# Optimization experiments

Measured on AMD Instinct MI355X. Metric: run time of the kernel, lower is better.

The kernel has to match this reference:

```python
import jax, jax.numpy as jnp
import numpy as np

B, NX, NY, NZ = 2, 64, 64, 64
D, CI, CO, F = 3, 32, 32, 64  # spatial dims, chan in/out, n_modes


def setup_inputs() -> dict:
    key = jax.random.key(0)
    ka, kx, ky, k1, k2, k3, k4, k5, k6 = jax.random.split(key, 9)
    omega, c = 30.0 / 300.0, 6.0
    u = lambda k, shape, scale: scale * (2.0 * jax.random.uniform(k, shape, jnp.float32) - 1.0)
    return {
        "a": jax.random.normal(ka, (B, NX, NY, NZ, CI), jnp.float32),
        "x": jax.random.uniform(kx, (B, NX, NY, NZ, D), jnp.float32),
        "y": jax.random.uniform(ky, (B, NX, NY, NZ, D), jnp.float32),
        "modes_a": u(k1, (F, CI), np.sqrt(c / (CI + F))),
        "modes_x": u(k2, (F, D), np.sqrt(c / (D + F)) * omega),
        "modes_y": u(k3, (F, D), np.sqrt(c / (D + F)) * omega),
        "modes_u": u(k4, (F, CO), np.sqrt(c / (F + CO))),
        "fc_w": jax.random.normal(k5, (CI, CO), jnp.float32) / np.sqrt(CI),
        "fc_b": jax.random.normal(k6, (CO,), jnp.float32) * 0.01,
    }


def reference(a, x, y, modes_a, modes_x, modes_y, modes_u, fc_w, fc_b):
    # SpectralAttention: Fourier-feature linear attention.
    # NOTE: source forward passes x for both coordinate args (att(h, x, x)).
    A = jnp.einsum('bxyzi,fi->bxyzf', a, modes_a)                       # [B,NX,NY,NZ,F]
    X = jnp.exp(-2j * np.pi * jnp.einsum('bxyzd,gd->bxyzg', x, modes_x))  # complex64
    Y = jnp.exp(2j * np.pi * jnp.einsum('bxyzd,gd->bxyzg', x, modes_y))   # complex64
    N = x.shape[1] * x.shape[2] * x.shape[3]
    AX = jnp.einsum('bxyzf,bxyzg->bfg', A.astype(X.dtype), X)           # [B,F,F] complex
    U = jnp.einsum('bfg,bxyzg->bxyzf', AX, Y).real / N                  # [B,NX,NY,NZ,F]
    u = jnp.einsum('bxyzf,fo->bxyzo', U, modes_u)                        # [B,NX,NY,NZ,CO]
    h = u + a @ fc_w + fc_b                                              # residual Linear
    return jax.nn.gelu(h)
```

## Files before the change

kernel.cpp:

```cpp
#include <hip/hip_runtime.h>
#include <math.h>

#define NB   2
#define NPTS 262144

typedef __attribute__((ext_vector_type(8))) __bf16 bf16x8;
typedef __attribute__((ext_vector_type(4))) float  f32x4;

__device__ __forceinline__ float gelu_fast(float v) {
    float t  = v * v;
    float z2 = v * (-2.302208f + -0.1029432f * t);
    float e  = __builtin_amdgcn_exp2f(z2);
    return v * __builtin_amdgcn_rcpf(1.0f + e);
}

__device__ __forceinline__ unsigned short bf16_rn(float f) {
    unsigned u = __builtin_bit_cast(unsigned, f);
    u += 0x7fffu + ((u >> 16) & 1u);
    return (unsigned short)(u >> 16);
}

template<bool WRITE_ABF>
__global__ __launch_bounds__(256)
void pass1_kernel(const float* __restrict__ a, const float* __restrict__ x,
                  const float* __restrict__ mx, float* __restrict__ part,
                  unsigned* __restrict__ abf, int NPB)
{
    __shared__ float4 xs[4][32];
    __shared__ float wsum[32 * 129];

    const int t = threadIdx.x, wave = t >> 6, lane = t & 63;
    const int l15 = lane & 15, l4 = lane >> 4;
    const int blk = blockIdx.x, b = blk / NPB, pb = blk % NPB;
    const int ppb = NPTS / NPB;
    const int chunks = ppb >> 5;
    const long base = (long)b * NPTS + (long)pb * ppb;

    float m0[4], m1[4], m2[4];
    #pragma unroll
    for (int ct = 0; ct < 4; ++ct) {
        int g = l15 + 16 * ct;
        m0[ct] = mx[g*3]; m1[ct] = mx[g*3+1]; m2[ct] = mx[g*3+2];
    }

    f32x4 acc[2][8];
    #pragma unroll
    for (int rt = 0; rt < 2; ++rt)
        #pragma unroll
        for (int ct = 0; ct < 8; ++ct)
            acc[rt][ct] = f32x4{0.f, 0.f, 0.f, 0.f};

    {
        const long p0 = base + ((long)wave << 5);
        if (lane < 32) {
            const float* xq = x + (p0 + lane) * 3;
            xs[wave][lane] = make_float4(xq[0], xq[1], xq[2], 0.f);
        }
    }
    float2 aq[8];
    {
        const long p0 = base + ((long)wave << 5);
        #pragma unroll
        for (int j = 0; j < 8; ++j)
            aq[j] = *(const float2*)(a + (p0 + l4*8 + j) * 32 + 2*l15);
    }

    for (int ci = wave; ci < chunks; ci += 4) {
        const long pc = base + ((long)ci << 5);
        const bool hasnext = (ci + 4) < chunks;
        const long pn = base + ((long)(ci + 4) << 5);

        bf16x8 afr[2];
        #pragma unroll
        for (int j = 0; j < 8; ++j) {
            unsigned short h0 = bf16_rn(aq[j].x);
            unsigned short h1 = bf16_rn(aq[j].y);
            if (WRITE_ABF)
                abf[(pc + l4*8 + j) * 16 + l15] = (unsigned)h0 | ((unsigned)h1 << 16);
            afr[0][j] = __builtin_bit_cast(__bf16, h0);
            afr[1][j] = __builtin_bit_cast(__bf16, h1);
        }

        float4 xp[8];
        #pragma unroll
        for (int j = 0; j < 8; ++j) xp[j] = xs[wave][l4*8 + j];

        float2 anq[8];
        if (hasnext) {
            #pragma unroll
            for (int j = 0; j < 8; ++j)
                anq[j] = *(const float2*)(a + (pn + l4*8 + j) * 32 + 2*l15);
            if (lane < 32) {
                const float* xq = x + (pn + lane) * 3;
                xs[wave][lane] = make_float4(xq[0], xq[1], xq[2], 0.f);
            }
        }

        #pragma unroll
        for (int ct = 0; ct < 4; ++ct) {
            bf16x8 bc, bs;
            #pragma unroll
            for (int j = 0; j < 8; ++j) {
                float d = xp[j].x*m0[ct] + xp[j].y*m1[ct] + xp[j].z*m2[ct];
                bc[j] = (__bf16)__builtin_amdgcn_cosf(d);
                bs[j] = (__bf16)__builtin_amdgcn_sinf(d);
            }
            #pragma unroll
            for (int rt = 0; rt < 2; ++rt) {
                acc[rt][ct]   = __builtin_amdgcn_mfma_f32_16x16x32_bf16(afr[rt], bc, acc[rt][ct],   0, 0, 0);
                acc[rt][ct+4] = __builtin_amdgcn_mfma_f32_16x16x32_bf16(afr[rt], bs, acc[rt][ct+4], 0, 0, 0);
            }
        }

        if (hasnext) {
            #pragma unroll
            for (int j = 0; j < 8; ++j) aq[j] = anq[j];
        }
    }

    for (int w = 0; w < 4; ++w) {
        if (wave == w) {
            #pragma unroll
            for (int rt = 0; rt < 2; ++rt)
                #pragma unroll
                for (int ct = 0; ct < 8; ++ct)
                    #pragma unroll
                    for (int r = 0; r < 4; ++r) {
                        int i = 2 * (l4*4 + r) + rt;
                        int c = ((ct & 3) * 16) + l15 + ((ct & 4) ? 64 : 0);
                        int id = i * 129 + c;
                        float v = acc[rt][ct][r];
                        if (w == 0) wsum[id] = v; else wsum[id] += v;
                    }
        }
        __syncthreads();
    }
    for (int idx = t; idx < 4096; idx += 256) {
        int i = idx >> 7, c = idx & 127;
        part[(long)blk * 4096 + idx] = wsum[i * 129 + c];
    }
}

__global__ __launch_bounds__(256)
void reduceW_kernel(const float* __restrict__ part, float* __restrict__ Wf, int NPB)
{
    __shared__ float red[8][33];
    const int t = threadIdx.x;
    const int b = blockIdx.x >> 7;
    const int jb = (blockIdx.x & 127) * 32;
    const int jj = jb + (t & 31), seg = t >> 5;
    const float* p = part + (long)b * NPB * 4096 + jj;
    float s = 0.f;
    for (int pb = seg; pb < NPB; pb += 8) s += p[(long)pb * 4096];
    red[seg][t & 31] = s;
    __syncthreads();
    if (t < 32) {
        float r = 0.f;
        #pragma unroll
        for (int q = 0; q < 8; ++q) r += red[q][t];
        Wf[b * 4096 + jb + t] = r;
    }
}

__global__ __launch_bounds__(256)
void vmat_kernel(const float* __restrict__ Wf, const float* __restrict__ ma,
                 const float* __restrict__ mu, const float* __restrict__ fcw,
                 unsigned short* __restrict__ Vb)
{
    __shared__ float Ws[4096];
    __shared__ float Qs[32][32];
    const int t = threadIdx.x, b = blockIdx.x;
    for (int i = t; i < 4096; i += 256) Ws[i] = Wf[b * 4096 + i];
    __syncthreads();
    for (int i = t; i < 1024; i += 256) {
        int o = i >> 5, ii = i & 31;
        float s = 0.f;
        for (int f = 0; f < 64; ++f) s += mu[f*32 + o] * ma[f*32 + ii];
        Qs[o][ii] = s;
    }
    __syncthreads();
    const float invN = 1.f / 262144.f;
    for (int i = t; i < 5120; i += 256) {
        int k = i >> 5, o = i & 31;
        float v;
        if (k < 128) {
            int g = k & 63, off = (k >= 64) ? 64 : 0;
            float s = 0.f;
            for (int q = 0; q < 32; ++q) s += Qs[o][q] * Ws[q*128 + off + g];
            v = s * invN;
        } else {
            v = fcw[(k - 128) * 32 + o];
        }
        Vb[b * 5120 + i] = bf16_rn(v);
    }
}

template<bool READ_ABF>
__global__ __launch_bounds__(256)
void pass2_kernel(const float* __restrict__ a, const unsigned* __restrict__ abf,
                  const float* __restrict__ x, const unsigned short* __restrict__ Vb,
                  const float* __restrict__ fcb, const float* __restrict__ my,
                  float* __restrict__ out)
{
    __shared__ float4 xs[4][32];
    __shared__ float4 mys[64];
    const int t = threadIdx.x, wave = t >> 6, lane = t & 63;
    const int l15 = lane & 15, l4 = lane >> 4;
    const int blk = blockIdx.x, b = blk >> 9, lb = blk & 511;
    const long base = (long)b * NPTS + (long)lb * 512;

    if (t < 64) { const float* mq = my + t*3; mys[t] = make_float4(mq[0], mq[1], mq[2], 0.f); }

    bf16x8 bfr[5][2];
    {
        const unsigned short* vb = Vb + b * 5120;
        #pragma unroll
        for (int c = 0; c < 5; ++c)
            #pragma unroll
            for (int ct = 0; ct < 2; ++ct) {
                bf16x8 tmp;
                #pragma unroll
                for (int j = 0; j < 8; ++j) {
                    unsigned short uv = vb[(32*c + l4*8 + j) * 32 + l15 + 16*ct];
                    tmp[j] = __builtin_bit_cast(__bf16, uv);
                }
                bfr[c][ct] = tmp;
            }
    }
    const float bias0 = fcb[l15], bias1 = fcb[l15 + 16];
    __syncthreads();

    {
        const long p0 = base + ((long)wave << 5);
        if (lane < 32) {
            const float* xq = x + (p0 + lane) * 3;
            xs[wave][lane] = make_float4(xq[0], xq[1], xq[2], 0.f);
        }
    }
    bf16x8 afr[2];
    {
        const long p0 = base + ((long)wave << 5);
        #pragma unroll
        for (int rt = 0; rt < 2; ++rt) {
            if (READ_ABF) {
                afr[rt] = __builtin_bit_cast(bf16x8,
                    *(const uint4*)(abf + (p0 + l15 + 16*rt) * 16 + l4*4));
            } else {
                const float* ap = a + (p0 + l15 + 16*rt) * 32 + l4*8;
                float4 a0 = *(const float4*)ap;
                float4 a1 = *(const float4*)(ap + 4);
                afr[rt][0] = (__bf16)a0.x; afr[rt][1] = (__bf16)a0.y;
                afr[rt][2] = (__bf16)a0.z; afr[rt][3] = (__bf16)a0.w;
                afr[rt][4] = (__bf16)a1.x; afr[rt][5] = (__bf16)a1.y;
                afr[rt][6] = (__bf16)a1.z; afr[rt][7] = (__bf16)a1.w;
            }
        }
    }

    for (int ci = wave; ci < 16; ci += 4) {
        const long pc = base + ((long)ci << 5);
        const bool hasnext = (ci + 4) < 16;
        const long pn = base + ((long)(ci + 4) << 5);

        float4 xp0 = xs[wave][l15];
        float4 xp1 = xs[wave][l15 + 16];

        bf16x8 anfr[2];
        if (hasnext) {
            #pragma unroll
            for (int rt = 0; rt < 2; ++rt) {
                if (READ_ABF) {
                    anfr[rt] = __builtin_bit_cast(bf16x8,
                        *(const uint4*)(abf + (pn + l15 + 16*rt) * 16 + l4*4));
                } else {
                    const float* ap = a + (pn + l15 + 16*rt) * 32 + l4*8;
                    float4 a0 = *(const float4*)ap;
                    float4 a1 = *(const float4*)(ap + 4);
                    anfr[rt][0] = (__bf16)a0.x; anfr[rt][1] = (__bf16)a0.y;
                    anfr[rt][2] = (__bf16)a0.z; anfr[rt][3] = (__bf16)a0.w;
                    anfr[rt][4] = (__bf16)a1.x; anfr[rt][5] = (__bf16)a1.y;
                    anfr[rt][6] = (__bf16)a1.z; anfr[rt][7] = (__bf16)a1.w;
                }
            }
            if (lane < 32) {
                const float* xq = x + (pn + lane) * 3;
                xs[wave][lane] = make_float4(xq[0], xq[1], xq[2], 0.f);
            }
        }

        f32x4 acc[2][2];
        #pragma unroll
        for (int rt = 0; rt < 2; ++rt)
            #pragma unroll
            for (int ct = 0; ct < 2; ++ct) acc[rt][ct] = f32x4{0.f,0.f,0.f,0.f};

        #pragma unroll
        for (int gt = 0; gt < 2; ++gt) {
            bf16x8 ac[2], as2[2];
            #pragma unroll
            for (int j = 0; j < 8; ++j) {
                float4 m = mys[gt*32 + l4*8 + j];
                float d0 = xp0.x*m.x + xp0.y*m.y + xp0.z*m.z;
                float d1 = xp1.x*m.x + xp1.y*m.y + xp1.z*m.z;
                ac[0][j]  = (__bf16)__builtin_amdgcn_cosf(d0);
                as2[0][j] = (__bf16)__builtin_amdgcn_sinf(d0);
                ac[1][j]  = (__bf16)__builtin_amdgcn_cosf(d1);
                as2[1][j] = (__bf16)__builtin_amdgcn_sinf(d1);
            }
            #pragma unroll
            for (int rt = 0; rt < 2; ++rt)
                #pragma unroll
                for (int ct = 0; ct < 2; ++ct) {
                    acc[rt][ct] = __builtin_amdgcn_mfma_f32_16x16x32_bf16(ac[rt],  bfr[gt][ct],   acc[rt][ct], 0, 0, 0);
                    acc[rt][ct] = __builtin_amdgcn_mfma_f32_16x16x32_bf16(as2[rt], bfr[2+gt][ct], acc[rt][ct], 0, 0, 0);
                }
        }
        #pragma unroll
        for (int rt = 0; rt < 2; ++rt)
            #pragma unroll
            for (int ct = 0; ct < 2; ++ct) {
                acc[rt][ct] = __builtin_amdgcn_mfma_f32_16x16x32_bf16(afr[rt], bfr[4][ct], acc[rt][ct], 0, 0, 0);
                float bias = ct ? bias1 : bias0;
                #pragma unroll
                for (int r = 0; r < 4; ++r) {
                    long p = pc + 16*rt + l4*4 + r;
                    out[p * 32 + l15 + 16*ct] = gelu_fast(acc[rt][ct][r] + bias);
                }
            }

        if (hasnext) { afr[0] = anfr[0]; afr[1] = anfr[1]; }
    }
}

extern "C" void kernel_launch(void* const* d_in, const int* in_sizes, int n_in,
                              void* d_out, int out_size, void* d_ws, size_t ws_size,
                              hipStream_t stream)
{
    const float* a   = (const float*)d_in[0];
    const float* x   = (const float*)d_in[1];
    const float* ma  = (const float*)d_in[3];
    const float* mx  = (const float*)d_in[4];
    const float* my  = (const float*)d_in[5];
    const float* mu  = (const float*)d_in[6];
    const float* fcw = (const float*)d_in[7];
    const float* fcb = (const float*)d_in[8];
    float* out = (float*)d_out;

    const size_t WfB  = (size_t)NB * 4096 * 4;
    const size_t VbB  = (size_t)NB * 5120 * 2;
    const size_t abfB = (size_t)NB * NPTS * 16 * 4;

    int NPB = 256;
    bool use_abf = ws_size >= (size_t)NB * NPB * 4096 * 4 + WfB + VbB + abfB + 256;
    if (!use_abf) {
        while (NPB > 32 &&
               ws_size < (size_t)NB * NPB * 4096 * 4 + WfB + VbB + 256)
            NPB >>= 1;
    }

    float* part = (float*)d_ws;
    float* Wf = part + (size_t)NB * NPB * 4096;
    unsigned short* Vb = (unsigned short*)(Wf + NB * 4096);
    unsigned* abf = (unsigned*)(Vb + NB * 5120);

    if (use_abf)
        pass1_kernel<true><<<NB * NPB, 256, 0, stream>>>(a, x, mx, part, abf, NPB);
    else
        pass1_kernel<false><<<NB * NPB, 256, 0, stream>>>(a, x, mx, part, abf, NPB);

    reduceW_kernel<<<NB * 128, 256, 0, stream>>>(part, Wf, NPB);
    vmat_kernel<<<NB, 256, 0, stream>>>(Wf, ma, mu, fcw, Vb);

    if (use_abf)
        pass2_kernel<true><<<NB * 512, 256, 0, stream>>>(a, abf, x, Vb, fcb, my, out);
    else
        pass2_kernel<false><<<NB * 512, 256, 0, stream>>>(a, abf, x, Vb, fcb, my, out);
}
```

Baseline: 83.20 us.

## Stage a-tile loads and output stores through LDS for coalesced float4 access

In pass1, each wave now loads its 32-point chunk of `a` with coalesced float4 reads into shared memory, then reads the bf16 fragments from LDS. This replaces the strided float2 global loads and drops the register prefetch of the next chunk. In pass2, gelu outputs are written to a per-wave LDS tile and then stored to global memory as float4 rows, replacing scattered scalar stores. The cost is extra LDS traffic and loss of software prefetch overlap in pass1. Pass1's LDS footprint also grows by 16KB, which may reduce occupancy.

Result: no change. 82.31 us (-1.1%).

```diff
diff --git a/kernel.cpp b/kernel.cpp
--- a/kernel.cpp
+++ b/kernel.cpp
@@ -28,6 +28,7 @@
 {
     __shared__ float4 xs[4][32];
     __shared__ float wsum[32 * 129];
+    __shared__ __align__(16) float atile[4][1024];
 
     const int t = threadIdx.x, wave = t >> 6, lane = t & 63;
     const int l15 = lane & 15, l4 = lane >> 4;
@@ -50,31 +51,25 @@
         for (int ct = 0; ct < 8; ++ct)
             acc[rt][ct] = f32x4{0.f, 0.f, 0.f, 0.f};
 
-    {
-        const long p0 = base + ((long)wave << 5);
-        if (lane < 32) {
-            const float* xq = x + (p0 + lane) * 3;
-            xs[wave][lane] = make_float4(xq[0], xq[1], xq[2], 0.f);
-        }
-    }
-    float2 aq[8];
-    {
-        const long p0 = base + ((long)wave << 5);
-        #pragma unroll
-        for (int j = 0; j < 8; ++j)
-            aq[j] = *(const float2*)(a + (p0 + l4*8 + j) * 32 + 2*l15);
-    }
-
     for (int ci = wave; ci < chunks; ci += 4) {
         const long pc = base + ((long)ci << 5);
-        const bool hasnext = (ci + 4) < chunks;
-        const long pn = base + ((long)(ci + 4) << 5);
+
+        if (lane < 32) {
+            const float* xq = x + (pc + lane) * 3;
+            xs[wave][lane] = make_float4(xq[0], xq[1], xq[2], 0.f);
+        }
+        #pragma unroll
+        for (int q = 0; q < 4; ++q) {
+            float4 v = *(const float4*)(a + pc * 32 + q * 256 + lane * 4);
+            *(float4*)&atile[wave][q * 256 + lane * 4] = v;
+        }
 
         bf16x8 afr[2];
         #pragma unroll
         for (int j = 0; j < 8; ++j) {
-            unsigned short h0 = bf16_rn(aq[j].x);
-            unsigned short h1 = bf16_rn(aq[j].y);
+            float2 av = *(const float2*)&atile[wave][(l4*8 + j) * 32 + 2*l15];
+            unsigned short h0 = bf16_rn(av.x);
+            unsigned short h1 = bf16_rn(av.y);
             if (WRITE_ABF)
                 abf[(pc + l4*8 + j) * 16 + l15] = (unsigned)h0 | ((unsigned)h1 << 16);
             afr[0][j] = __builtin_bit_cast(__bf16, h0);
@@ -85,17 +80,6 @@
         #pragma unroll
         for (int j = 0; j < 8; ++j) xp[j] = xs[wave][l4*8 + j];
 
-        float2 anq[8];
-        if (hasnext) {
-            #pragma unroll
-            for (int j = 0; j < 8; ++j)
-                anq[j] = *(const float2*)(a + (pn + l4*8 + j) * 32 + 2*l15);
-            if (lane < 32) {
-                const float* xq = x + (pn + lane) * 3;
-                xs[wave][lane] = make_float4(xq[0], xq[1], xq[2], 0.f);
-            }
-        }
-
         #pragma unroll
         for (int ct = 0; ct < 4; ++ct) {
             bf16x8 bc, bs;
@@ -110,11 +94,6 @@
                 acc[rt][ct]   = __builtin_amdgcn_mfma_f32_16x16x32_bf16(afr[rt], bc, acc[rt][ct],   0, 0, 0);
                 acc[rt][ct+4] = __builtin_amdgcn_mfma_f32_16x16x32_bf16(afr[rt], bs, acc[rt][ct+4], 0, 0, 0);
             }
-        }
-
-        if (hasnext) {
-            #pragma unroll
-            for (int j = 0; j < 8; ++j) aq[j] = anq[j];
         }
     }
 
@@ -204,6 +183,7 @@
 {
     __shared__ float4 xs[4][32];
     __shared__ float4 mys[64];
+    __shared__ __align__(16) float st[4][16][32];
     const int t = threadIdx.x, wave = t >> 6, lane = t & 63;
     const int l15 = lane & 15, l4 = lane >> 4;
     const int blk = blockIdx.x, b = blk >> 9, lb = blk & 511;
@@ -316,17 +296,24 @@
                 }
         }
         #pragma unroll
-        for (int rt = 0; rt < 2; ++rt)
+        for (int rt = 0; rt < 2; ++rt) {
             #pragma unroll
             for (int ct = 0; ct < 2; ++ct) {
                 acc[rt][ct] = __builtin_amdgcn_mfma_f32_16x16x32_bf16(afr[rt], bfr[4][ct], acc[rt][ct], 0, 0, 0);
                 float bias = ct ? bias1 : bias0;
                 #pragma unroll
-                for (int r = 0; r < 4; ++r) {
-                    long p = pc + 16*rt + l4*4 + r;
-                    out[p * 32 + l15 + 16*ct] = gelu_fast(acc[rt][ct][r] + bias);
-                }
-            }
+                for (int r = 0; r < 4; ++r)
+                    st[wave][l4*4 + r][l15 + 16*ct] = gelu_fast(acc[rt][ct][r] + bias);
+            }
+            {
+                int row = lane >> 3;
+                int c4  = (lane & 7) * 4;
+                float4 v0 = *(const float4*)&st[wave][row][c4];
+                float4 v1 = *(const float4*)&st[wave][row + 8][c4];
+                *(float4*)&out[(pc + 16*rt + row) * 32 + c4]     = v0;
+                *(float4*)&out[(pc + 16*rt + row + 8) * 32 + c4] = v1;
+            }
+        }
 
         if (hasnext) { afr[0] = anfr[0]; afr[1] = anfr[1]; }
     }
```
